# Kernel optimization log

Measured on AMD Instinct MI355X. Metric: run time of the kernel, lower is better.

Reference implementation:

```python
import jax, jax.numpy as jnp
import numpy as np

N_NODES = 50000
N_EDGES = 400000
D_PROT = 512
D_TEXT = 2048
GN_EPS = 1e-5


def setup_inputs() -> dict:
    key = jax.random.key(0)
    ks = jax.random.split(key, 8)
    s = 0.02
    return {
        "x": jax.random.normal(ks[0], (N_NODES, D_PROT), jnp.float32),
        "edge_index": jax.random.randint(ks[1], (2, N_EDGES), 0, N_NODES, dtype=jnp.int32),
        "gn_weight": jnp.ones((D_PROT,), jnp.float32),
        "gn_bias": jnp.zeros((D_PROT,), jnp.float32),
        "gn_mean_scale": jnp.ones((D_PROT,), jnp.float32),
        "conv1_w": jax.random.normal(ks[2], (D_PROT, D_PROT), jnp.float32) * s,
        "conv1_b": jnp.zeros((D_PROT,), jnp.float32),
        "conv2_w": jax.random.normal(ks[3], (D_PROT, D_PROT), jnp.float32) * s,
        "conv2_b": jnp.zeros((D_PROT,), jnp.float32),
        "proj1_w": jax.random.normal(ks[4], (D_TEXT, D_PROT), jnp.float32) * s,
        "proj1_b": jnp.zeros((D_TEXT,), jnp.float32),
        "proj2_w": jax.random.normal(ks[5], (D_TEXT, D_TEXT), jnp.float32) * s,
        "proj2_b": jnp.zeros((D_TEXT,), jnp.float32),
    }


def _graph_norm(x, weight, bias, mean_scale):
    # PyG GraphNorm over a single graph: shift by mean_scale*mean, scale by rstd
    mean = jnp.mean(x, axis=0, keepdims=True)            # [1, D]
    out = x - mean * mean_scale
    var = jnp.mean(out * out, axis=0, keepdims=True)     # [1, D]
    out = out * jax.lax.rsqrt(var + GN_EPS)
    return out * weight + bias


def _sgconv(x, src, dst, w, b):
    # SGConv K=1 with GCN normalization and added self-loops:
    n = x.shape[0]
    deg = jax.ops.segment_sum(jnp.ones_like(src, dtype=x.dtype), dst, num_segments=n) + 1.0
    dinv = jax.lax.rsqrt(deg)                            # [N]
    norm = dinv[src] * dinv[dst]                         # [E]
    agg = jax.ops.segment_sum(x[src] * norm[:, None], dst, num_segments=n)
    agg = agg + x * (dinv * dinv)[:, None]               # self-loop contribution
    return agg @ w.T + b


def reference(x, edge_index, gn_weight, gn_bias, gn_mean_scale,
              conv1_w, conv1_b, conv2_w, conv2_b,
              proj1_w, proj1_b, proj2_w, proj2_b):
    src, dst = edge_index[0], edge_index[1]
    h = _graph_norm(x, gn_weight, gn_bias, gn_mean_scale)
    h = jax.nn.relu(_sgconv(h, src, dst, conv1_w, conv1_b))  # dropout = identity (eval)
    h = jax.nn.relu(_sgconv(h, src, dst, conv2_w, conv2_b))
    h = h @ proj1_w.T + proj1_b
    h = jax.nn.gelu(h, approximate=False)
    h = h @ proj2_w.T + proj2_b
    return h
```

## Files before the change

### kernel.cpp

```cpp
#include <hip/hip_runtime.h>
#include <math.h>

typedef _Float16 half_t;
typedef _Float16 f16x2 __attribute__((ext_vector_type(2)));
typedef _Float16 f16x4 __attribute__((ext_vector_type(4)));
typedef _Float16 f16x8 __attribute__((ext_vector_type(8)));
typedef float f32x4 __attribute__((ext_vector_type(4)));

#define D_PROT 512
#define D_TEXT 2048

__global__ void k_cvt4(const float* __restrict__ s, half_t* __restrict__ d, int n4) {
    int i = blockIdx.x * 256 + threadIdx.x;
    if (i < n4) {
        float4 v = ((const float4*)s)[i];
        f16x4 o;
        o.x = (_Float16)v.x; o.y = (_Float16)v.y;
        o.z = (_Float16)v.z; o.w = (_Float16)v.w;
        ((f16x4*)d)[i] = o;
    }
}

__global__ void k_deg(const int* __restrict__ dst, int E, int* __restrict__ deg) {
    int i = blockIdx.x * 256 + threadIdx.x;
    if (i < E) atomicAdd(&deg[dst[i]], 1);
}

__global__ void k_dinv(const int* __restrict__ deg, float* __restrict__ dinv, int n) {
    int i = blockIdx.x * 256 + threadIdx.x;
    if (i < n) dinv[i] = rsqrtf((float)deg[i] + 1.0f);
}

__global__ void k_blocksum(const int* __restrict__ deg, int* __restrict__ bsum, int n) {
    __shared__ int sd[256];
    int i = blockIdx.x * 256 + threadIdx.x;
    sd[threadIdx.x] = (i < n) ? deg[i] : 0;
    __syncthreads();
    for (int s = 128; s > 0; s >>= 1) {
        if (threadIdx.x < s) sd[threadIdx.x] += sd[threadIdx.x + s];
        __syncthreads();
    }
    if (threadIdx.x == 0) bsum[blockIdx.x] = sd[0];
}

__global__ void k_scan_bsum(const int* __restrict__ bsum, int* __restrict__ boff, int nb) {
    if (threadIdx.x == 0 && blockIdx.x == 0) {
        int acc = 0;
        for (int i = 0; i < nb; i++) { boff[i] = acc; acc += bsum[i]; }
    }
}

__global__ void k_scan_final(const int* __restrict__ deg, const int* __restrict__ boff,
                             int* __restrict__ rowptr, int n) {
    __shared__ int sd[256];
    int i = blockIdx.x * 256 + threadIdx.x;
    int v = (i < n) ? deg[i] : 0;
    sd[threadIdx.x] = v;
    __syncthreads();
    for (int s = 1; s < 256; s <<= 1) {
        int t2 = (threadIdx.x >= s) ? sd[threadIdx.x - s] : 0;
        __syncthreads();
        sd[threadIdx.x] += t2;
        __syncthreads();
    }
    if (i < n) rowptr[i + 1] = boff[blockIdx.x] + sd[threadIdx.x];
}

__global__ void k_fill(const int* __restrict__ src, const int* __restrict__ dst, int E,
                       const int* __restrict__ rowptr, int* __restrict__ fill,
                       int* __restrict__ colidx) {
    int i = blockIdx.x * 256 + threadIdx.x;
    if (i < E) {
        int d = dst[i];
        int pos = atomicAdd(&fill[d], 1);
        colidx[rowptr[d] + pos] = src[i];
    }
}

__global__ void k_gnreduce(const float* __restrict__ x, float* __restrict__ sums,
                           float* __restrict__ sumsq, int Nn) {
    int t = threadIdx.x;
    int c = t * 2;
    float s0 = 0, s1 = 0, q0 = 0, q1 = 0;
    for (int r = blockIdx.x; r < Nn; r += gridDim.x) {
        float2 v = *(const float2*)(x + (size_t)r * D_PROT + c);
        s0 += v.x; s1 += v.y; q0 += v.x * v.x; q1 += v.y * v.y;
    }
    atomicAdd(&sums[c], s0);  atomicAdd(&sums[c + 1], s1);
    atomicAdd(&sumsq[c], q0); atomicAdd(&sumsq[c + 1], q1);
}

__global__ void k_gnfinal(const float* __restrict__ sums, const float* __restrict__ sumsq,
                          const float* __restrict__ w, const float* __restrict__ b,
                          const float* __restrict__ ms, float* __restrict__ ab, float invN) {
    int d = blockIdx.x * 256 + threadIdx.x;
    if (d < D_PROT) {
        float mean = sums[d] * invN;
        float m2 = sumsq[d] * invN;
        float mm = mean * ms[d];
        float var = m2 - 2.f * mm * mean + mm * mm;
        float rstd = rsqrtf(var + 1e-5f);
        float a = rstd * w[d];
        ab[d] = a;
        ab[D_PROT + d] = b[d] - mm * a;
    }
}

__global__ void k_gnnorm(const float* __restrict__ x, const float* __restrict__ ab,
                         half_t* __restrict__ h, int n4) {
    int i = blockIdx.x * 256 + threadIdx.x;
    if (i < n4) {
        size_t idx = (size_t)i * 4;
        float4 v = *(const float4*)(x + idx);
        int d = (int)(idx & (D_PROT - 1));
        const float* a = ab;
        const float* bb = ab + D_PROT;
        f16x4 o;
        o.x = (_Float16)(v.x * a[d]     + bb[d]);
        o.y = (_Float16)(v.y * a[d + 1] + bb[d + 1]);
        o.z = (_Float16)(v.z * a[d + 2] + bb[d + 2]);
        o.w = (_Float16)(v.w * a[d + 3] + bb[d + 3]);
        *(f16x4*)(h + idx) = o;
    }
}

__global__ void k_agg(const half_t* __restrict__ h, half_t* __restrict__ out,
                      const int* __restrict__ rowptr, const int* __restrict__ colidx,
                      const float* __restrict__ dinv) {
    int node = blockIdx.x;
    int t = threadIdx.x;
    float di = dinv[node];
    int beg = rowptr[node], end = rowptr[node + 1];
    f16x2 sv = ((const f16x2*)(h + (size_t)node * D_PROT))[t];
    float dii = di * di;
    float a0 = (float)sv.x * dii, a1 = (float)sv.y * dii;
    for (int e = beg; e < end; ++e) {
        int s = colidx[e];
        float wgt = dinv[s] * di;
        f16x2 v = ((const f16x2*)(h + (size_t)s * D_PROT))[t];
        a0 += wgt * (float)v.x;
        a1 += wgt * (float)v.y;
    }
    f16x2 o; o.x = (_Float16)a0; o.y = (_Float16)a1;
    ((f16x2*)(out + (size_t)node * D_PROT))[t] = o;
}

#define FENCE() asm volatile("" ::: "memory")
#define BAR()   do { FENCE(); __builtin_amdgcn_s_barrier(); FENCE(); } while (0)
#define WAITV4() asm volatile("s_waitcnt vmcnt(4)" ::: "memory")
#define WAITV0() asm volatile("s_waitcnt vmcnt(0)" ::: "memory")
#define GLD(src, dst) __builtin_amdgcn_global_load_lds( \
    (const __attribute__((address_space(1))) void*)(src), \
    (__attribute__((address_space(3))) void*)(dst), 16, 0, 0)
#define LDF(base, row, kk) \
    (*(const f16x8*)((base) + ((((row) * 128 + (kk) * 64 + fqo)) ^ (((row) & 7) << 4))))
#define MM(mi, nj, A_, B_) \
    acc[mi][nj] = __builtin_amdgcn_mfma_f32_16x16x32_f16(A_, B_, acc[mi][nj], 0, 0, 0)

template <int ACT, typename OUT_T>
__global__ __launch_bounds__(512, 2) void k_gemm8(const half_t* __restrict__ A,
                                                  const half_t* __restrict__ W,
                                                  const float* __restrict__ bias,
                                                  OUT_T* __restrict__ C,
                                                  int M, int N, int K) {
    __shared__ half_t sm[2][32768];
    const int gx = gridDim.x;
    const int nwg = gx * gridDim.y;
    int b = blockIdx.y * gx + blockIdx.x;
    int w8 = ((nwg & 7) == 0) ? (b & 7) * (nwg >> 3) + (b >> 3) : b;
    const int bn = (w8 % gx) * 256;
    const int bm = (w8 / gx) * 256;

    const int t = threadIdx.x;
    const int w = t >> 6, lane = t & 63;
    const int fr = lane & 15, fq = lane >> 4;
    const int fqo = fq * 16;
    const int wm = (w >> 2) * 128, wn = (w & 3) * 64;
    const int NT = K >> 6;

    int q0 = w * 512 + lane * 8;
    int q1 = 4096 + q0;
    int s0 = q0 ^ (((q0 >> 6) & 7) << 3);
    int s1 = q1 ^ (((q1 >> 6) & 7) << 3);
    int r0 = s0 >> 6, c0 = s0 & 63;
    int r1 = s1 >> 6, c1 = s1 & 63;
    const half_t* gAlo0 = A + (size_t)min(bm + r0, M - 1) * K + c0;
    const half_t* gAlo1 = A + (size_t)min(bm + r1, M - 1) * K + c1;
    const half_t* gAhi0 = A + (size_t)min(bm + 128 + r0, M - 1) * K + c0;
    const half_t* gAhi1 = A + (size_t)min(bm + 128 + r1, M - 1) * K + c1;
    const half_t* gBlo0 = W + (size_t)(bn + r0) * K + c0;
    const half_t* gBlo1 = W + (size_t)(bn + r1) * K + c1;
    const half_t* gBhi0 = W + (size_t)(bn + 128 + r0) * K + c0;
    const half_t* gBhi1 = W + (size_t)(bn + 128 + r1) * K + c1;
    const int dst0 = w * 512;

    f32x4 acc[8][4] = {};

    GLD(gAlo0, &sm[0][dst0]);          GLD(gAlo1, &sm[0][4096 + dst0]);
    GLD(gAhi0, &sm[0][8192 + dst0]);   GLD(gAhi1, &sm[0][12288 + dst0]);
    GLD(gBlo0, &sm[0][16384 + dst0]);  GLD(gBlo1, &sm[0][20480 + dst0]);
    GLD(gBhi0, &sm[0][24576 + dst0]);  GLD(gBhi1, &sm[0][28672 + dst0]);
    GLD(gBlo0 + 64, &sm[1][16384 + dst0]);  GLD(gBlo1 + 64, &sm[1][20480 + dst0]);
    GLD(gBhi0 + 64, &sm[1][24576 + dst0]);  GLD(gBhi1 + 64, &sm[1][28672 + dst0]);
    WAITV4();
    BAR();

#define TILE(cur, nxt, ktA, ktB) do {                                          \
    const char* smA = (const char*)&sm[cur][0];                                 \
    const char* smB = (const char*)&sm[cur][16384];                             \
                  \
    f16x8 b00 = LDF(smB, wn + fr, 0),      b01 = LDF(smB, wn + fr, 1);          \
    f16x8 b10 = LDF(smB, wn + 16 + fr, 0), b11 = LDF(smB, wn + 16 + fr, 1);     \
    f16x8 b20 = LDF(smB, wn + 32 + fr, 0), b21 = LDF(smB, wn + 32 + fr, 1);     \
    f16x8 b30 = LDF(smB, wn + 48 + fr, 0), b31 = LDF(smB, wn + 48 + fr, 1);     \
    f16x8 a00 = LDF(smA, wm + fr, 0),      a01 = LDF(smA, wm + fr, 1);          \
    f16x8 a10 = LDF(smA, wm + 16 + fr, 0), a11 = LDF(smA, wm + 16 + fr, 1);     \
    GLD(gAlo0 + (size_t)(ktA) * 64, &sm[nxt][dst0]);                            \
    GLD(gAlo1 + (size_t)(ktA) * 64, &sm[nxt][4096 + dst0]);                     \
    GLD(gAhi0 + (size_t)(ktA) * 64, &sm[nxt][8192 + dst0]);                     \
    GLD(gAhi1 + (size_t)(ktA) * 64, &sm[nxt][12288 + dst0]);                    \
    BAR();                                                                      \
    __builtin_amdgcn_s_setprio(1);                                              \
    MM(0, 0, a00, b00); MM(0, 1, a00, b10); MM(0, 2, a00, b20); MM(0, 3, a00, b30); \
    MM(0, 0, a01, b01); MM(0, 1, a01, b11); MM(0, 2, a01, b21); MM(0, 3, a01, b31); \
    MM(1, 0, a10, b00); MM(1, 1, a10, b10); MM(1, 2, a10, b20); MM(1, 3, a10, b30); \
    MM(1, 0, a11, b01); MM(1, 1, a11, b11); MM(1, 2, a11, b21); MM(1, 3, a11, b31); \
    __builtin_amdgcn_s_setprio(0);                                              \
    BAR();                                                                      \
                              \
    f16x8 a20 = LDF(smA, wm + 32 + fr, 0), a21 = LDF(smA, wm + 32 + fr, 1);     \
    f16x8 a30 = LDF(smA, wm + 48 + fr, 0), a31 = LDF(smA, wm + 48 + fr, 1);     \
    GLD(gBlo0 + (size_t)(ktB) * 64, &sm[cur][16384 + dst0]);                    \
    GLD(gBlo1 + (size_t)(ktB) * 64, &sm[cur][20480 + dst0]);                    \
    BAR();                                                                      \
    __builtin_amdgcn_s_setprio(1);                                              \
    MM(2, 0, a20, b00); MM(2, 1, a20, b10); MM(2, 2, a20, b20); MM(2, 3, a20, b30); \
    MM(2, 0, a21, b01); MM(2, 1, a21, b11); MM(2, 2, a21, b21); MM(2, 3, a21, b31); \
    MM(3, 0, a30, b00); MM(3, 1, a30, b10); MM(3, 2, a30, b20); MM(3, 3, a30, b30); \
    MM(3, 0, a31, b01); MM(3, 1, a31, b11); MM(3, 2, a31, b21); MM(3, 3, a31, b31); \
    __builtin_amdgcn_s_setprio(0);                                              \
    BAR();                                                                      \
                              \
    f16x8 a40 = LDF(smA, wm + 64 + fr, 0), a41 = LDF(smA, wm + 64 + fr, 1);     \
    f16x8 a50 = LDF(smA, wm + 80 + fr, 0), a51 = LDF(smA, wm + 80 + fr, 1);     \
    GLD(gBhi0 + (size_t)(ktB) * 64, &sm[cur][24576 + dst0]);                    \
    GLD(gBhi1 + (size_t)(ktB) * 64, &sm[cur][28672 + dst0]);                    \
    BAR();                                                                      \
    __builtin_amdgcn_s_setprio(1);                                              \
    MM(4, 0, a40, b00); MM(4, 1, a40, b10); MM(4, 2, a40, b20); MM(4, 3, a40, b30); \
    MM(4, 0, a41, b01); MM(4, 1, a41, b11); MM(4, 2, a41, b21); MM(4, 3, a41, b31); \
    MM(5, 0, a50, b00); MM(5, 1, a50, b10); MM(5, 2, a50, b20); MM(5, 3, a50, b30); \
    MM(5, 0, a51, b01); MM(5, 1, a51, b11); MM(5, 2, a51, b21); MM(5, 3, a51, b31); \
    __builtin_amdgcn_s_setprio(0);                                              \
    BAR();                                                                      \
                  \
    f16x8 a60 = LDF(smA, wm + 96 + fr, 0),  a61 = LDF(smA, wm + 96 + fr, 1);    \
    f16x8 a70 = LDF(smA, wm + 112 + fr, 0), a71 = LDF(smA, wm + 112 + fr, 1);   \
    BAR();                                                                      \
    __builtin_amdgcn_s_setprio(1);                                              \
    MM(6, 0, a60, b00); MM(6, 1, a60, b10); MM(6, 2, a60, b20); MM(6, 3, a60, b30); \
    MM(6, 0, a61, b01); MM(6, 1, a61, b11); MM(6, 2, a61, b21); MM(6, 3, a61, b31); \
    MM(7, 0, a70, b00); MM(7, 1, a70, b10); MM(7, 2, a70, b20); MM(7, 3, a70, b30); \
    MM(7, 0, a71, b01); MM(7, 1, a71, b11); MM(7, 2, a71, b21); MM(7, 3, a71, b31); \
    __builtin_amdgcn_s_setprio(0);                                              \
    WAITV4();                                                                   \
    BAR();                                                                      \
} while (0)

    for (int tt = 0; tt < NT; tt += 2) {
        int kb1 = (tt + 2 < NT) ? tt + 2 : NT - 1;
        TILE(0, 1, tt + 1, kb1);
        int ka2 = (tt + 2 < NT) ? tt + 2 : NT - 1;
        int kb2 = (tt + 3 < NT) ? tt + 3 : NT - 1;
        TILE(1, 0, ka2, kb2);
    }
    WAITV0();
#undef TILE

    const int col0 = bn + wn + fr;
#pragma unroll
    for (int mi = 0; mi < 8; mi++) {
        int rb = bm + wm + mi * 16 + fq * 4;
#pragma unroll
        for (int nj = 0; nj < 4; nj++) {
            int col = col0 + nj * 16;
            float bv = bias[col];
#pragma unroll
            for (int r = 0; r < 4; r++) {
                int row = rb + r;
                if (row < M) {
                    float v = acc[mi][nj][r] + bv;
                    if (ACT == 1) v = fmaxf(v, 0.f);
                    if (ACT == 2) v = 0.5f * v * (1.f + erff(v * 0.70710678118f));
                    C[(size_t)row * N + col] = (OUT_T)v;
                }
            }
        }
    }
}

extern "C" void kernel_launch(void* const* d_in, const int* in_sizes, int n_in,
                              void* d_out, int out_size, void* d_ws, size_t ws_size,
                              hipStream_t stream) {
    const float* x     = (const float*)d_in[0];
    const int*   eidx  = (const int*)d_in[1];
    const float* gn_w  = (const float*)d_in[2];
    const float* gn_b  = (const float*)d_in[3];
    const float* gn_ms = (const float*)d_in[4];
    const float* w1    = (const float*)d_in[5];
    const float* b1    = (const float*)d_in[6];
    const float* w2    = (const float*)d_in[7];
    const float* b2    = (const float*)d_in[8];
    const float* p1    = (const float*)d_in[9];
    const float* pb1   = (const float*)d_in[10];
    const float* p2    = (const float*)d_in[11];
    const float* pb2   = (const float*)d_in[12];

    const int Nn = in_sizes[0] / D_PROT;
    const int E  = in_sizes[1] / 2;
    const int M  = Nn;

    char* ws = (char*)d_ws;
    size_t off = 0;
    auto alloc = [&](size_t bytes) {
        void* p = ws + off;
        off += (bytes + 255) & ~(size_t)255;
        return p;
    };
    half_t* w1h    = (half_t*)alloc((size_t)D_PROT * D_PROT * 2);
    half_t* w2h    = (half_t*)alloc((size_t)D_PROT * D_PROT * 2);
    half_t* p1h    = (half_t*)alloc((size_t)D_TEXT * D_PROT * 2);
    half_t* p2h    = (half_t*)alloc((size_t)D_TEXT * D_TEXT * 2);
    int*    deg    = (int*)alloc((size_t)Nn * 4);
    float*  dinv   = (float*)alloc((size_t)Nn * 4);
    int*    rowptr = (int*)alloc((size_t)(Nn + 1) * 4);
    int*    fillc  = (int*)alloc((size_t)Nn * 4);
    int*    bsum   = (int*)alloc(1024);
    int*    boff   = (int*)alloc(1024);
    int*    colidx = (int*)alloc((size_t)E * 4);
    float*  sums   = (float*)alloc(D_PROT * 4);
    float*  sumsq  = (float*)alloc(D_PROT * 4);
    float*  gnab   = (float*)alloc(2 * D_PROT * 4);
    half_t* buf1   = (half_t*)alloc((size_t)Nn * D_PROT * 2);
    half_t* buf2   = (half_t*)alloc((size_t)Nn * D_PROT * 2);
    half_t* big    = (half_t*)alloc((size_t)Nn * D_TEXT * 2);

    const int* esrc = eidx;
    const int* edst = eidx + E;

    hipMemsetAsync(deg, 0, (size_t)Nn * 4, stream);
    hipMemsetAsync(fillc, 0, (size_t)Nn * 4, stream);
    hipMemsetAsync(rowptr, 0, (size_t)(Nn + 1) * 4, stream);
    hipMemsetAsync(sums, 0, D_PROT * 4, stream);
    hipMemsetAsync(sumsq, 0, D_PROT * 4, stream);

    k_cvt4<<<(D_PROT * D_PROT / 4 + 255) / 256, 256, 0, stream>>>(w1, w1h, D_PROT * D_PROT / 4);
    k_cvt4<<<(D_PROT * D_PROT / 4 + 255) / 256, 256, 0, stream>>>(w2, w2h, D_PROT * D_PROT / 4);
    k_cvt4<<<(D_TEXT * D_PROT / 4 + 255) / 256, 256, 0, stream>>>(p1, p1h, D_TEXT * D_PROT / 4);
    k_cvt4<<<(D_TEXT * D_TEXT / 4 + 255) / 256, 256, 0, stream>>>(p2, p2h, D_TEXT * D_TEXT / 4);

    int eb = (E + 255) / 256;
    int nb = (Nn + 255) / 256;
    k_deg<<<eb, 256, 0, stream>>>(edst, E, deg);
    k_dinv<<<nb, 256, 0, stream>>>(deg, dinv, Nn);
    k_blocksum<<<nb, 256, 0, stream>>>(deg, bsum, Nn);
    k_scan_bsum<<<1, 1, 0, stream>>>(bsum, boff, nb);
    k_scan_final<<<nb, 256, 0, stream>>>(deg, boff, rowptr, Nn);
    k_fill<<<eb, 256, 0, stream>>>(esrc, edst, E, rowptr, fillc, colidx);

    k_gnreduce<<<256, 256, 0, stream>>>(x, sums, sumsq, Nn);
    k_gnfinal<<<2, 256, 0, stream>>>(sums, sumsq, gn_w, gn_b, gn_ms, gnab, 1.0f / (float)Nn);
    int n4 = Nn * D_PROT / 4;
    k_gnnorm<<<(n4 + 255) / 256, 256, 0, stream>>>(x, gnab, buf1, n4);

    const int mt256 = (M + 255) / 256;

    k_agg<<<Nn, 256, 0, stream>>>(buf1, buf2, rowptr, colidx, dinv);
    {
        dim3 g(D_PROT / 256, mt256);
        k_gemm8<1, half_t><<<g, 512, 0, stream>>>(buf2, w1h, b1, buf1, M, D_PROT, D_PROT);
    }
    k_agg<<<Nn, 256, 0, stream>>>(buf1, buf2, rowptr, colidx, dinv);
    {
        dim3 g(D_PROT / 256, mt256);
        k_gemm8<1, half_t><<<g, 512, 0, stream>>>(buf2, w2h, b2, buf1, M, D_PROT, D_PROT);
    }
    {
        dim3 g(D_TEXT / 256, mt256);
        k_gemm8<2, half_t><<<g, 512, 0, stream>>>(buf1, p1h, pb1, big, M, D_TEXT, D_PROT);
    }
    {
        dim3 g(D_TEXT / 256, mt256);
        k_gemm8<0, float><<<g, 512, 0, stream>>>(big, p2h, pb2, (float*)d_out, M, D_TEXT, D_TEXT);
    }
}
```

Measured before the change: 1.321 ms.

## Vectorize SpMM aggregation with 4-edge unroll and restructure GEMM double-buffer pipeline

The aggregation kernel now uses 128 threads per node, each handling four halves, and unrolls the edge loop by four so several neighbor gathers are in flight at once. The GEMM main loop is rewritten as a simpler single-tile-per-iteration double buffer. It loads all A/B fragments from LDS up front, issues the full next-stage global-to-LDS copy mid-tile, and waits with vmcnt(8). This cuts barriers per tile from eight to two, at the cost of higher register pressure from holding all 16 A fragments live.

```diff
diff --git a/kernel.cpp b/kernel.cpp
--- a/kernel.cpp
+++ b/kernel.cpp
@@ -131,24 +131,41 @@
     int t = threadIdx.x;
     float di = dinv[node];
     int beg = rowptr[node], end = rowptr[node + 1];
-    f16x2 sv = ((const f16x2*)(h + (size_t)node * D_PROT))[t];
+    const f16x4* hp = (const f16x4*)h;
+    f16x4 sv = hp[node * 128 + t];
     float dii = di * di;
     float a0 = (float)sv.x * dii, a1 = (float)sv.y * dii;
-    for (int e = beg; e < end; ++e) {
+    float a2 = (float)sv.z * dii, a3 = (float)sv.w * dii;
+    int e = beg;
+    for (; e + 4 <= end; e += 4) {
+        int s0 = colidx[e],     s1 = colidx[e + 1];
+        int s2 = colidx[e + 2], s3 = colidx[e + 3];
+        float w0 = dinv[s0] * di, w1 = dinv[s1] * di;
+        float w2 = dinv[s2] * di, w3 = dinv[s3] * di;
+        f16x4 v0 = hp[s0 * 128 + t], v1 = hp[s1 * 128 + t];
+        f16x4 v2 = hp[s2 * 128 + t], v3 = hp[s3 * 128 + t];
+        a0 += w0 * (float)v0.x + w1 * (float)v1.x + w2 * (float)v2.x + w3 * (float)v3.x;
+        a1 += w0 * (float)v0.y + w1 * (float)v1.y + w2 * (float)v2.y + w3 * (float)v3.y;
+        a2 += w0 * (float)v0.z + w1 * (float)v1.z + w2 * (float)v2.z + w3 * (float)v3.z;
+        a3 += w0 * (float)v0.w + w1 * (float)v1.w + w2 * (float)v2.w + w3 * (float)v3.w;
+    }
+    for (; e < end; ++e) {
         int s = colidx[e];
         float wgt = dinv[s] * di;
-        f16x2 v = ((const f16x2*)(h + (size_t)s * D_PROT))[t];
-        a0 += wgt * (float)v.x;
-        a1 += wgt * (float)v.y;
-    }
-    f16x2 o; o.x = (_Float16)a0; o.y = (_Float16)a1;
-    ((f16x2*)(out + (size_t)node * D_PROT))[t] = o;
+        f16x4 v = hp[s * 128 + t];
+        a0 += wgt * (float)v.x; a1 += wgt * (float)v.y;
+        a2 += wgt * (float)v.z; a3 += wgt * (float)v.w;
+    }
+    f16x4 o;
+    o.x = (_Float16)a0; o.y = (_Float16)a1; o.z = (_Float16)a2; o.w = (_Float16)a3;
+    ((f16x4*)out)[node * 128 + t] = o;
 }
 
 #define FENCE() asm volatile("" ::: "memory")
 #define BAR()   do { FENCE(); __builtin_amdgcn_s_barrier(); FENCE(); } while (0)
-#define WAITV4() asm volatile("s_waitcnt vmcnt(4)" ::: "memory")
+#define WAITV8() asm volatile("s_waitcnt vmcnt(8)" ::: "memory")
 #define WAITV0() asm volatile("s_waitcnt vmcnt(0)" ::: "memory")
+#define LGKM0()  asm volatile("s_waitcnt lgkmcnt(0)" ::: "memory")
 #define GLD(src, dst) __builtin_amdgcn_global_load_lds( \
     (const __attribute__((address_space(1))) void*)(src), \
     (__attribute__((address_space(3))) void*)(dst), 16, 0, 0)
@@ -194,88 +211,72 @@
     const half_t* gBhi1 = W + (size_t)(bn + 128 + r1) * K + c1;
     const int dst0 = w * 512;
 
+#define STAGE(cur, kt) do {                                                    \
+    GLD(gAlo0 + (size_t)(kt) * 64, &sm[cur][dst0]);                            \
+    GLD(gAlo1 + (size_t)(kt) * 64, &sm[cur][4096 + dst0]);                     \
+    GLD(gAhi0 + (size_t)(kt) * 64, &sm[cur][8192 + dst0]);                     \
+    GLD(gAhi1 + (size_t)(kt) * 64, &sm[cur][12288 + dst0]);                    \
+    GLD(gBlo0 + (size_t)(kt) * 64, &sm[cur][16384 + dst0]);                    \
+    GLD(gBlo1 + (size_t)(kt) * 64, &sm[cur][20480 + dst0]);                    \
+    GLD(gBhi0 + (size_t)(kt) * 64, &sm[cur][24576 + dst0]);                    \
+    GLD(gBhi1 + (size_t)(kt) * 64, &sm[cur][28672 + dst0]);                    \
+} while (0)
+
     f32x4 acc[8][4] = {};
 
-    GLD(gAlo0, &sm[0][dst0]);          GLD(gAlo1, &sm[0][4096 + dst0]);
-    GLD(gAhi0, &sm[0][8192 + dst0]);   GLD(gAhi1, &sm[0][12288 + dst0]);
-    GLD(gBlo0, &sm[0][16384 + dst0]);  GLD(gBlo1, &sm[0][20480 + dst0]);
-    GLD(gBhi0, &sm[0][24576 + dst0]);  GLD(gBhi1, &sm[0][28672 + dst0]);
-    GLD(gBlo0 + 64, &sm[1][16384 + dst0]);  GLD(gBlo1 + 64, &sm[1][20480 + dst0]);
-    GLD(gBhi0 + 64, &sm[1][24576 + dst0]);  GLD(gBhi1 + 64, &sm[1][28672 + dst0]);
-    WAITV4();
+    STAGE(0, 0);
+    STAGE(1, (NT > 1 ? 1 : 0));
+    WAITV8();
     BAR();
 
-#define TILE(cur, nxt, ktA, ktB) do {                                          \
-    const char* smA = (const char*)&sm[cur][0];                                 \
-    const char* smB = (const char*)&sm[cur][16384];                             \
-                  \
-    f16x8 b00 = LDF(smB, wn + fr, 0),      b01 = LDF(smB, wn + fr, 1);          \
-    f16x8 b10 = LDF(smB, wn + 16 + fr, 0), b11 = LDF(smB, wn + 16 + fr, 1);     \
-    f16x8 b20 = LDF(smB, wn + 32 + fr, 0), b21 = LDF(smB, wn + 32 + fr, 1);     \
-    f16x8 b30 = LDF(smB, wn + 48 + fr, 0), b31 = LDF(smB, wn + 48 + fr, 1);     \
-    f16x8 a00 = LDF(smA, wm + fr, 0),      a01 = LDF(smA, wm + fr, 1);          \
-    f16x8 a10 = LDF(smA, wm + 16 + fr, 0), a11 = LDF(smA, wm + 16 + fr, 1);     \
-    GLD(gAlo0 + (size_t)(ktA) * 64, &sm[nxt][dst0]);                            \
-    GLD(gAlo1 + (size_t)(ktA) * 64, &sm[nxt][4096 + dst0]);                     \
-    GLD(gAhi0 + (size_t)(ktA) * 64, &sm[nxt][8192 + dst0]);                     \
-    GLD(gAhi1 + (size_t)(ktA) * 64, &sm[nxt][12288 + dst0]);                    \
-    BAR();                                                                      \
-    __builtin_amdgcn_s_setprio(1);                                              \
-    MM(0, 0, a00, b00); MM(0, 1, a00, b10); MM(0, 2, a00, b20); MM(0, 3, a00, b30); \
-    MM(0, 0, a01, b01); MM(0, 1, a01, b11); MM(0, 2, a01, b21); MM(0, 3, a01, b31); \
-    MM(1, 0, a10, b00); MM(1, 1, a10, b10); MM(1, 2, a10, b20); MM(1, 3, a10, b30); \
-    MM(1, 0, a11, b01); MM(1, 1, a11, b11); MM(1, 2, a11, b21); MM(1, 3, a11, b31); \
-    __builtin_amdgcn_s_setprio(0);                                              \
-    BAR();                                                                      \
-                              \
-    f16x8 a20 = LDF(smA, wm + 32 + fr, 0), a21 = LDF(smA, wm + 32 + fr, 1);     \
-    f16x8 a30 = LDF(smA, wm + 48 + fr, 0), a31 = LDF(smA, wm + 48 + fr, 1);     \
-    GLD(gBlo0 + (size_t)(ktB) * 64, &sm[cur][16384 + dst0]);                    \
-    GLD(gBlo1 + (size_t)(ktB) * 64, &sm[cur][20480 + dst0]);                    \
-    BAR();                                                                      \
-    __builtin_amdgcn_s_setprio(1);                                              \
-    MM(2, 0, a20, b00); MM(2, 1, a20, b10); MM(2, 2, a20, b20); MM(2, 3, a20, b30); \
-    MM(2, 0, a21, b01); MM(2, 1, a21, b11); MM(2, 2, a21, b21); MM(2, 3, a21, b31); \
-    MM(3, 0, a30, b00); MM(3, 1, a30, b10); MM(3, 2, a30, b20); MM(3, 3, a30, b30); \
-    MM(3, 0, a31, b01); MM(3, 1, a31, b11); MM(3, 2, a31, b21); MM(3, 3, a31, b31); \
-    __builtin_amdgcn_s_setprio(0);                                              \
-    BAR();                                                                      \
-                              \
-    f16x8 a40 = LDF(smA, wm + 64 + fr, 0), a41 = LDF(smA, wm + 64 + fr, 1);     \
-    f16x8 a50 = LDF(smA, wm + 80 + fr, 0), a51 = LDF(smA, wm + 80 + fr, 1);     \
-    GLD(gBhi0 + (size_t)(ktB) * 64, &sm[cur][24576 + dst0]);                    \
-    GLD(gBhi1 + (size_t)(ktB) * 64, &sm[cur][28672 + dst0]);                    \
-    BAR();                                                                      \
-    __builtin_amdgcn_s_setprio(1);                                              \
-    MM(4, 0, a40, b00); MM(4, 1, a40, b10); MM(4, 2, a40, b20); MM(4, 3, a40, b30); \
-    MM(4, 0, a41, b01); MM(4, 1, a41, b11); MM(4, 2, a41, b21); MM(4, 3, a41, b31); \
-    MM(5, 0, a50, b00); MM(5, 1, a50, b10); MM(5, 2, a50, b20); MM(5, 3, a50, b30); \
-    MM(5, 0, a51, b01); MM(5, 1, a51, b11); MM(5, 2, a51, b21); MM(5, 3, a51, b31); \
-    __builtin_amdgcn_s_setprio(0);                                              \
-    BAR();                                                                      \
-                  \
-    f16x8 a60 = LDF(smA, wm + 96 + fr, 0),  a61 = LDF(smA, wm + 96 + fr, 1);    \
-    f16x8 a70 = LDF(smA, wm + 112 + fr, 0), a71 = LDF(smA, wm + 112 + fr, 1);   \
-    BAR();                                                                      \
-    __builtin_amdgcn_s_setprio(1);                                              \
-    MM(6, 0, a60, b00); MM(6, 1, a60, b10); MM(6, 2, a60, b20); MM(6, 3, a60, b30); \
-    MM(6, 0, a61, b01); MM(6, 1, a61, b11); MM(6, 2, a61, b21); MM(6, 3, a61, b31); \
-    MM(7, 0, a70, b00); MM(7, 1, a70, b10); MM(7, 2, a70, b20); MM(7, 3, a70, b30); \
-    MM(7, 0, a71, b01); MM(7, 1, a71, b11); MM(7, 2, a71, b21); MM(7, 3, a71, b31); \
-    __builtin_amdgcn_s_setprio(0);                                              \
-    WAITV4();                                                                   \
-    BAR();                                                                      \
-} while (0)
-
-    for (int tt = 0; tt < NT; tt += 2) {
-        int kb1 = (tt + 2 < NT) ? tt + 2 : NT - 1;
-        TILE(0, 1, tt + 1, kb1);
-        int ka2 = (tt + 2 < NT) ? tt + 2 : NT - 1;
-        int kb2 = (tt + 3 < NT) ? tt + 3 : NT - 1;
-        TILE(1, 0, ka2, kb2);
+    for (int tt = 0; tt < NT; ++tt) {
+        const int cur = tt & 1;
+        const char* smA = (const char*)&sm[cur][0];
+        const char* smB = (const char*)&sm[cur][16384];
+
+        f16x8 bf[4][2], af[8][2];
+#pragma unroll
+        for (int nj = 0; nj < 4; nj++) {
+            bf[nj][0] = LDF(smB, wn + nj * 16 + fr, 0);
+            bf[nj][1] = LDF(smB, wn + nj * 16 + fr, 1);
+        }
+#pragma unroll
+        for (int mi = 0; mi < 2; mi++) {
+            af[mi][0] = LDF(smA, wm + mi * 16 + fr, 0);
+            af[mi][1] = LDF(smA, wm + mi * 16 + fr, 1);
+        }
+#pragma unroll
+        for (int mi = 2; mi < 8; mi++) {
+            af[mi][0] = LDF(smA, wm + mi * 16 + fr, 0);
+            af[mi][1] = LDF(smA, wm + mi * 16 + fr, 1);
+        }
+        __builtin_amdgcn_s_setprio(1);
+#pragma unroll
+        for (int mi = 0; mi < 2; mi++)
+#pragma unroll
+            for (int nj = 0; nj < 4; nj++) {
+                MM(mi, nj, af[mi][0], bf[nj][0]);
+                MM(mi, nj, af[mi][1], bf[nj][1]);
+            }
+        __builtin_amdgcn_s_setprio(0);
+        LGKM0();
+        BAR();
+        int kt = (tt + 2 < NT) ? tt + 2 : NT - 1;
+        STAGE(cur, kt);
+        __builtin_amdgcn_s_setprio(1);
+#pragma unroll
+        for (int mi = 2; mi < 8; mi++)
+#pragma unroll
+            for (int nj = 0; nj < 4; nj++) {
+                MM(mi, nj, af[mi][0], bf[nj][0]);
+                MM(mi, nj, af[mi][1], bf[nj][1]);
+            }
+        __builtin_amdgcn_s_setprio(0);
+        WAITV8();
+        BAR();
     }
     WAITV0();
-#undef TILE
+#undef STAGE
 
     const int col0 = bn + wn + fr;
 #pragma unroll
@@ -375,12 +376,12 @@
 
     const int mt256 = (M + 255) / 256;
 
-    k_agg<<<Nn, 256, 0, stream>>>(buf1, buf2, rowptr, colidx, dinv);
+    k_agg<<<Nn, 128, 0, stream>>>(buf1, buf2, rowptr, colidx, dinv);
     {
         dim3 g(D_PROT / 256, mt256);
         k_gemm8<1, half_t><<<g, 512, 0, stream>>>(buf2, w1h, b1, buf1, M, D_PROT, D_PROT);
     }
-    k_agg<<<Nn, 256, 0, stream>>>(buf1, buf2, rowptr, colidx, dinv);
+    k_agg<<<Nn, 128, 0, stream>>>(buf1, buf2, rowptr, colidx, dinv);
     {
         dim3 g(D_PROT / 256, mt256);
         k_gemm8<1, half_t><<<g, 512, 0, stream>>>(buf2, w2h, b2, buf1, M, D_PROT, D_PROT);
```

After: 1.458 ms. 10.4% more time.

## Vectorize and unroll SpMM gather, drop GEMM swizzle, respread global loads

Applied to the files above, without the earlier changes.

The aggregation kernel now has each of 128 threads handle four fp16 features and unrolls the edge loop by four, so more independent gathers are in flight per thread. The GEMM drops the XCD-aware block remapping in favour of direct blockIdx mapping. It also spreads the next-tile A and B global-to-LDS loads evenly across the four sub-phases of each tile instead of batching them. Removing the remap may hurt L2 locality across chiplets, and the new load schedule changes vmcnt accounting against the existing WAITV4.

```diff
diff --git a/kernel.cpp b/kernel.cpp
--- a/kernel.cpp
+++ b/kernel.cpp
@@ -131,18 +131,34 @@
     int t = threadIdx.x;
     float di = dinv[node];
     int beg = rowptr[node], end = rowptr[node + 1];
-    f16x2 sv = ((const f16x2*)(h + (size_t)node * D_PROT))[t];
+    const f16x4* hp = (const f16x4*)h;
+    f16x4 sv = hp[node * 128 + t];
     float dii = di * di;
     float a0 = (float)sv.x * dii, a1 = (float)sv.y * dii;
-    for (int e = beg; e < end; ++e) {
+    float a2 = (float)sv.z * dii, a3 = (float)sv.w * dii;
+    int e = beg;
+    for (; e + 4 <= end; e += 4) {
+        int s0 = colidx[e],     s1 = colidx[e + 1];
+        int s2 = colidx[e + 2], s3 = colidx[e + 3];
+        float w0 = dinv[s0] * di, w1 = dinv[s1] * di;
+        float w2 = dinv[s2] * di, w3 = dinv[s3] * di;
+        f16x4 v0 = hp[s0 * 128 + t], v1 = hp[s1 * 128 + t];
+        f16x4 v2 = hp[s2 * 128 + t], v3 = hp[s3 * 128 + t];
+        a0 += w0 * (float)v0.x + w1 * (float)v1.x + w2 * (float)v2.x + w3 * (float)v3.x;
+        a1 += w0 * (float)v0.y + w1 * (float)v1.y + w2 * (float)v2.y + w3 * (float)v3.y;
+        a2 += w0 * (float)v0.z + w1 * (float)v1.z + w2 * (float)v2.z + w3 * (float)v3.z;
+        a3 += w0 * (float)v0.w + w1 * (float)v1.w + w2 * (float)v2.w + w3 * (float)v3.w;
+    }
+    for (; e < end; ++e) {
         int s = colidx[e];
         float wgt = dinv[s] * di;
-        f16x2 v = ((const f16x2*)(h + (size_t)s * D_PROT))[t];
-        a0 += wgt * (float)v.x;
-        a1 += wgt * (float)v.y;
-    }
-    f16x2 o; o.x = (_Float16)a0; o.y = (_Float16)a1;
-    ((f16x2*)(out + (size_t)node * D_PROT))[t] = o;
+        f16x4 v = hp[s * 128 + t];
+        a0 += wgt * (float)v.x; a1 += wgt * (float)v.y;
+        a2 += wgt * (float)v.z; a3 += wgt * (float)v.w;
+    }
+    f16x4 o;
+    o.x = (_Float16)a0; o.y = (_Float16)a1; o.z = (_Float16)a2; o.w = (_Float16)a3;
+    ((f16x4*)out)[node * 128 + t] = o;
 }
 
 #define FENCE() asm volatile("" ::: "memory")
@@ -164,12 +180,8 @@
                                                   OUT_T* __restrict__ C,
                                                   int M, int N, int K) {
     __shared__ half_t sm[2][32768];
-    const int gx = gridDim.x;
-    const int nwg = gx * gridDim.y;
-    int b = blockIdx.y * gx + blockIdx.x;
-    int w8 = ((nwg & 7) == 0) ? (b & 7) * (nwg >> 3) + (b >> 3) : b;
-    const int bn = (w8 % gx) * 256;
-    const int bm = (w8 / gx) * 256;
+    const int bn = blockIdx.x * 256;
+    const int bm = blockIdx.y * 256;
 
     const int t = threadIdx.x;
     const int w = t >> 6, lane = t & 63;
@@ -194,31 +206,46 @@
     const half_t* gBhi1 = W + (size_t)(bn + 128 + r1) * K + c1;
     const int dst0 = w * 512;
 
+#define STAGE_ALO(buf, kt) do {                                                \
+    GLD(gAlo0 + (size_t)(kt) * 64, &sm[buf][dst0]);                            \
+    GLD(gAlo1 + (size_t)(kt) * 64, &sm[buf][4096 + dst0]);                     \
+} while (0)
+#define STAGE_AHI(buf, kt) do {                                                \
+    GLD(gAhi0 + (size_t)(kt) * 64, &sm[buf][8192 + dst0]);                     \
+    GLD(gAhi1 + (size_t)(kt) * 64, &sm[buf][12288 + dst0]);                    \
+} while (0)
+#define STAGE_BLO(buf, kt) do {                                                \
+    GLD(gBlo0 + (size_t)(kt) * 64, &sm[buf][16384 + dst0]);                    \
+    GLD(gBlo1 + (size_t)(kt) * 64, &sm[buf][20480 + dst0]);                    \
+} while (0)
+#define STAGE_BHI(buf, kt) do {                                                \
+    GLD(gBhi0 + (size_t)(kt) * 64, &sm[buf][24576 + dst0]);                    \
+    GLD(gBhi1 + (size_t)(kt) * 64, &sm[buf][28672 + dst0]);                    \
+} while (0)
+
     f32x4 acc[8][4] = {};
 
-    GLD(gAlo0, &sm[0][dst0]);          GLD(gAlo1, &sm[0][4096 + dst0]);
-    GLD(gAhi0, &sm[0][8192 + dst0]);   GLD(gAhi1, &sm[0][12288 + dst0]);
-    GLD(gBlo0, &sm[0][16384 + dst0]);  GLD(gBlo1, &sm[0][20480 + dst0]);
-    GLD(gBhi0, &sm[0][24576 + dst0]);  GLD(gBhi1, &sm[0][28672 + dst0]);
-    GLD(gBlo0 + 64, &sm[1][16384 + dst0]);  GLD(gBlo1 + 64, &sm[1][20480 + dst0]);
-    GLD(gBhi0 + 64, &sm[1][24576 + dst0]);  GLD(gBhi1 + 64, &sm[1][28672 + dst0]);
+    STAGE_ALO(0, 0); STAGE_AHI(0, 0); STAGE_BLO(0, 0); STAGE_BHI(0, 0);
+    {
+        int k1 = (NT > 1) ? 1 : 0;
+        STAGE_BLO(1, k1); STAGE_BHI(1, k1);
+    }
     WAITV4();
     BAR();
 
-#define TILE(cur, nxt, ktA, ktB) do {                                          \
+#define TILE(cur, nxt, tt) do {                                                 \
     const char* smA = (const char*)&sm[cur][0];                                 \
     const char* smB = (const char*)&sm[cur][16384];                             \
-                  \
+    const int kA = ((tt) + 1 < NT) ? (tt) + 1 : NT - 1;                         \
+    const int kB = ((tt) + 2 < NT) ? (tt) + 2 : NT - 1;                         \
+                        \
     f16x8 b00 = LDF(smB, wn + fr, 0),      b01 = LDF(smB, wn + fr, 1);          \
     f16x8 b10 = LDF(smB, wn + 16 + fr, 0), b11 = LDF(smB, wn + 16 + fr, 1);     \
     f16x8 b20 = LDF(smB, wn + 32 + fr, 0), b21 = LDF(smB, wn + 32 + fr, 1);     \
     f16x8 b30 = LDF(smB, wn + 48 + fr, 0), b31 = LDF(smB, wn + 48 + fr, 1);     \
     f16x8 a00 = LDF(smA, wm + fr, 0),      a01 = LDF(smA, wm + fr, 1);          \
     f16x8 a10 = LDF(smA, wm + 16 + fr, 0), a11 = LDF(smA, wm + 16 + fr, 1);     \
-    GLD(gAlo0 + (size_t)(ktA) * 64, &sm[nxt][dst0]);                            \
-    GLD(gAlo1 + (size_t)(ktA) * 64, &sm[nxt][4096 + dst0]);                     \
-    GLD(gAhi0 + (size_t)(ktA) * 64, &sm[nxt][8192 + dst0]);                     \
-    GLD(gAhi1 + (size_t)(ktA) * 64, &sm[nxt][12288 + dst0]);                    \
+    STAGE_ALO(nxt, kA);                                                         \
     BAR();                                                                      \
     __builtin_amdgcn_s_setprio(1);                                              \
     MM(0, 0, a00, b00); MM(0, 1, a00, b10); MM(0, 2, a00, b20); MM(0, 3, a00, b30); \
@@ -227,11 +254,10 @@
     MM(1, 0, a11, b01); MM(1, 1, a11, b11); MM(1, 2, a11, b21); MM(1, 3, a11, b31); \
     __builtin_amdgcn_s_setprio(0);                                              \
     BAR();                                                                      \
-                              \
+                                \
     f16x8 a20 = LDF(smA, wm + 32 + fr, 0), a21 = LDF(smA, wm + 32 + fr, 1);     \
     f16x8 a30 = LDF(smA, wm + 48 + fr, 0), a31 = LDF(smA, wm + 48 + fr, 1);     \
-    GLD(gBlo0 + (size_t)(ktB) * 64, &sm[cur][16384 + dst0]);                    \
-    GLD(gBlo1 + (size_t)(ktB) * 64, &sm[cur][20480 + dst0]);                    \
+    STAGE_AHI(nxt, kA);                                                         \
     BAR();                                                                      \
     __builtin_amdgcn_s_setprio(1);                                              \
     MM(2, 0, a20, b00); MM(2, 1, a20, b10); MM(2, 2, a20, b20); MM(2, 3, a20, b30); \
@@ -240,11 +266,10 @@
     MM(3, 0, a31, b01); MM(3, 1, a31, b11); MM(3, 2, a31, b21); MM(3, 3, a31, b31); \
     __builtin_amdgcn_s_setprio(0);                                              \
     BAR();                                                                      \
-                              \
+                                \
     f16x8 a40 = LDF(smA, wm + 64 + fr, 0), a41 = LDF(smA, wm + 64 + fr, 1);     \
     f16x8 a50 = LDF(smA, wm + 80 + fr, 0), a51 = LDF(smA, wm + 80 + fr, 1);     \
-    GLD(gBhi0 + (size_t)(ktB) * 64, &sm[cur][24576 + dst0]);                    \
-    GLD(gBhi1 + (size_t)(ktB) * 64, &sm[cur][28672 + dst0]);                    \
+    STAGE_BLO(cur, kB);                                                         \
     BAR();                                                                      \
     __builtin_amdgcn_s_setprio(1);                                              \
     MM(4, 0, a40, b00); MM(4, 1, a40, b10); MM(4, 2, a40, b20); MM(4, 3, a40, b30); \
@@ -256,6 +281,7 @@
                   \
     f16x8 a60 = LDF(smA, wm + 96 + fr, 0),  a61 = LDF(smA, wm + 96 + fr, 1);    \
     f16x8 a70 = LDF(smA, wm + 112 + fr, 0), a71 = LDF(smA, wm + 112 + fr, 1);   \
+    STAGE_BHI(cur, kB);                                                         \
     BAR();                                                                      \
     __builtin_amdgcn_s_setprio(1);                                              \
     MM(6, 0, a60, b00); MM(6, 1, a60, b10); MM(6, 2, a60, b20); MM(6, 3, a60, b30); \
@@ -268,14 +294,15 @@
 } while (0)
 
     for (int tt = 0; tt < NT; tt += 2) {
-        int kb1 = (tt + 2 < NT) ? tt + 2 : NT - 1;
-        TILE(0, 1, tt + 1, kb1);
-        int ka2 = (tt + 2 < NT) ? tt + 2 : NT - 1;
-        int kb2 = (tt + 3 < NT) ? tt + 3 : NT - 1;
-        TILE(1, 0, ka2, kb2);
+        TILE(0, 1, tt);
+        TILE(1, 0, tt + 1);
     }
     WAITV0();
 #undef TILE
+#undef STAGE_ALO
+#undef STAGE_AHI
+#undef STAGE_BLO
+#undef STAGE_BHI
 
     const int col0 = bn + wn + fr;
 #pragma unroll
@@ -375,12 +402,12 @@
 
     const int mt256 = (M + 255) / 256;
 
-    k_agg<<<Nn, 256, 0, stream>>>(buf1, buf2, rowptr, colidx, dinv);
+    k_agg<<<Nn, 128, 0, stream>>>(buf1, buf2, rowptr, colidx, dinv);
     {
         dim3 g(D_PROT / 256, mt256);
         k_gemm8<1, half_t><<<g, 512, 0, stream>>>(buf2, w1h, b1, buf1, M, D_PROT, D_PROT);
     }
-    k_agg<<<Nn, 256, 0, stream>>>(buf1, buf2, rowptr, colidx, dinv);
+    k_agg<<<Nn, 128, 0, stream>>>(buf1, buf2, rowptr, colidx, dinv);
     {
         dim3 g(D_PROT / 256, mt256);
         k_gemm8<1, half_t><<<g, 512, 0, stream>>>(buf2, w2h, b2, buf1, M, D_PROT, D_PROT);
```

After: 1.253 ms. 5.2% less time.

## Assign one wavefront per node in aggregation and parallelize block-offset scan

Applied to the files above, without the earlier changes.

The SpMM aggregation kernel now handles one node per 64-lane wavefront with 16-byte f16x8 loads, unrolled four edges at a time. Previously it used a 256-thread block per node with 4-byte loads. This cuts per-block overhead and raises memory-level parallelism on the gather. The single-thread serial scan of block sums becomes a 256-thread shared-memory Hillis-Steele scan, and the bsum/boff buffers grow to 4096 bytes.

```diff
diff --git a/kernel.cpp b/kernel.cpp
--- a/kernel.cpp
+++ b/kernel.cpp
@@ -44,10 +44,23 @@
 }
 
 __global__ void k_scan_bsum(const int* __restrict__ bsum, int* __restrict__ boff, int nb) {
-    if (threadIdx.x == 0 && blockIdx.x == 0) {
-        int acc = 0;
-        for (int i = 0; i < nb; i++) { boff[i] = acc; acc += bsum[i]; }
-    }
+    __shared__ int sd[1024];
+    int t = threadIdx.x;
+    for (int i = t; i < 1024; i += 256) sd[i] = (i < nb) ? bsum[i] : 0;
+    __syncthreads();
+    for (int s = 1; s < 1024; s <<= 1) {
+        int vals[4];
+#pragma unroll
+        for (int k = 0; k < 4; k++) {
+            int i = t + k * 256;
+            vals[k] = (i >= s) ? sd[i - s] : 0;
+        }
+        __syncthreads();
+#pragma unroll
+        for (int k = 0; k < 4; k++) sd[t + k * 256] += vals[k];
+        __syncthreads();
+    }
+    for (int i = t; i < nb; i += 256) boff[i] = (i > 0) ? sd[i - 1] : 0;
 }
 
 __global__ void k_scan_final(const int* __restrict__ deg, const int* __restrict__ boff,
@@ -126,23 +139,45 @@
 
 __global__ void k_agg(const half_t* __restrict__ h, half_t* __restrict__ out,
                       const int* __restrict__ rowptr, const int* __restrict__ colidx,
-                      const float* __restrict__ dinv) {
-    int node = blockIdx.x;
-    int t = threadIdx.x;
+                      const float* __restrict__ dinv, int Nn) {
+    int wid = (blockIdx.x << 2) + (threadIdx.x >> 6);
+    if (wid >= Nn) return;
+    int lane = threadIdx.x & 63;
+    int node = wid;
     float di = dinv[node];
     int beg = rowptr[node], end = rowptr[node + 1];
-    f16x2 sv = ((const f16x2*)(h + (size_t)node * D_PROT))[t];
+    const f16x8* hp = (const f16x8*)h;
+    f16x8 sv = hp[(size_t)node * 64 + lane];
     float dii = di * di;
-    float a0 = (float)sv.x * dii, a1 = (float)sv.y * dii;
-    for (int e = beg; e < end; ++e) {
+    float a[8];
+#pragma unroll
+    for (int j = 0; j < 8; j++) a[j] = (float)sv[j] * dii;
+    int e = beg;
+    for (; e + 4 <= end; e += 4) {
+        int s0 = colidx[e],     s1 = colidx[e + 1];
+        int s2 = colidx[e + 2], s3 = colidx[e + 3];
+        float w0 = dinv[s0] * di, w1 = dinv[s1] * di;
+        float w2 = dinv[s2] * di, w3 = dinv[s3] * di;
+        f16x8 v0 = hp[(size_t)s0 * 64 + lane];
+        f16x8 v1 = hp[(size_t)s1 * 64 + lane];
+        f16x8 v2 = hp[(size_t)s2 * 64 + lane];
+        f16x8 v3 = hp[(size_t)s3 * 64 + lane];
+#pragma unroll
+        for (int j = 0; j < 8; j++)
+            a[j] += w0 * (float)v0[j] + w1 * (float)v1[j]
+                  + w2 * (float)v2[j] + w3 * (float)v3[j];
+    }
+    for (; e < end; ++e) {
         int s = colidx[e];
-        float wgt = dinv[s] * di;
-        f16x2 v = ((const f16x2*)(h + (size_t)s * D_PROT))[t];
-        a0 += wgt * (float)v.x;
-        a1 += wgt * (float)v.y;
-    }
-    f16x2 o; o.x = (_Float16)a0; o.y = (_Float16)a1;
-    ((f16x2*)(out + (size_t)node * D_PROT))[t] = o;
+        float wg = dinv[s] * di;
+        f16x8 v = hp[(size_t)s * 64 + lane];
+#pragma unroll
+        for (int j = 0; j < 8; j++) a[j] += wg * (float)v[j];
+    }
+    f16x8 o;
+#pragma unroll
+    for (int j = 0; j < 8; j++) o[j] = (_Float16)a[j];
+    ((f16x8*)out)[(size_t)node * 64 + lane] = o;
 }
 
 #define FENCE() asm volatile("" ::: "memory")
@@ -253,7 +288,7 @@
     MM(5, 0, a51, b01); MM(5, 1, a51, b11); MM(5, 2, a51, b21); MM(5, 3, a51, b31); \
     __builtin_amdgcn_s_setprio(0);                                              \
     BAR();                                                                      \
-                  \
+                                       \
     f16x8 a60 = LDF(smA, wm + 96 + fr, 0),  a61 = LDF(smA, wm + 96 + fr, 1);    \
     f16x8 a70 = LDF(smA, wm + 112 + fr, 0), a71 = LDF(smA, wm + 112 + fr, 1);   \
     BAR();                                                                      \
@@ -335,8 +370,8 @@
     float*  dinv   = (float*)alloc((size_t)Nn * 4);
     int*    rowptr = (int*)alloc((size_t)(Nn + 1) * 4);
     int*    fillc  = (int*)alloc((size_t)Nn * 4);
-    int*    bsum   = (int*)alloc(1024);
-    int*    boff   = (int*)alloc(1024);
+    int*    bsum   = (int*)alloc(4096);
+    int*    boff   = (int*)alloc(4096);
     int*    colidx = (int*)alloc((size_t)E * 4);
     float*  sums   = (float*)alloc(D_PROT * 4);
     float*  sumsq  = (float*)alloc(D_PROT * 4);
@@ -364,7 +399,7 @@
     k_deg<<<eb, 256, 0, stream>>>(edst, E, deg);
     k_dinv<<<nb, 256, 0, stream>>>(deg, dinv, Nn);
     k_blocksum<<<nb, 256, 0, stream>>>(deg, bsum, Nn);
-    k_scan_bsum<<<1, 1, 0, stream>>>(bsum, boff, nb);
+    k_scan_bsum<<<1, 256, 0, stream>>>(bsum, boff, nb);
     k_scan_final<<<nb, 256, 0, stream>>>(deg, boff, rowptr, Nn);
     k_fill<<<eb, 256, 0, stream>>>(esrc, edst, E, rowptr, fillc, colidx);
 
@@ -374,13 +409,14 @@
     k_gnnorm<<<(n4 + 255) / 256, 256, 0, stream>>>(x, gnab, buf1, n4);
 
     const int mt256 = (M + 255) / 256;
-
-    k_agg<<<Nn, 256, 0, stream>>>(buf1, buf2, rowptr, colidx, dinv);
+    const int aggb = (Nn + 3) / 4;
+
+    k_agg<<<aggb, 256, 0, stream>>>(buf1, buf2, rowptr, colidx, dinv, Nn);
     {
         dim3 g(D_PROT / 256, mt256);
         k_gemm8<1, half_t><<<g, 512, 0, stream>>>(buf2, w1h, b1, buf1, M, D_PROT, D_PROT);
     }
-    k_agg<<<Nn, 256, 0, stream>>>(buf1, buf2, rowptr, colidx, dinv);
+    k_agg<<<aggb, 256, 0, stream>>>(buf1, buf2, rowptr, colidx, dinv, Nn);
     {
         dim3 g(D_PROT / 256, mt256);
         k_gemm8<1, half_t><<<g, 512, 0, stream>>>(buf2, w2h, b2, buf1, M, D_PROT, D_PROT);
```

Result: faster. 1.249 ms (-5.5%).
